# Kernel tuning notes

Measured on AMD Instinct MI355X. Metric: run time of the kernel, lower is better.

The kernel has to match this reference:

```python
import jax, jax.numpy as jnp
import numpy as np

H, W, C, E = 6, 40, 512, 128  # hardcoded in module


def setup_inputs() -> dict:
    key = jax.random.key(0)
    ks = jax.random.split(key, 9)
    nB = 512
    inp = {
        "prev_hidden": jax.random.normal(ks[0], (nB, C), jnp.float32),
        "conv_feats": jax.random.normal(ks[1], (nB, C, H, W), jnp.float32),
        "conv_feats_origin": jax.random.normal(ks[2], (nB, C, H, W), jnp.float32),
        "cur_embeddings": jax.random.normal(ks[3], (nB, E), jnp.float32),
        # params
        "score_w": jax.random.normal(ks[4], (C,), jnp.float32) * (1.0 / np.sqrt(C)),
        "w_ih": jax.random.normal(ks[5], (3 * C, C + E), jnp.float32) * (1.0 / np.sqrt(C)),
        "w_hh": jax.random.normal(ks[6], (3 * C, C), jnp.float32) * (1.0 / np.sqrt(C)),
        "b_ih": jax.random.normal(ks[7], (3 * C,), jnp.float32) * 0.01,
        "b_hh": jax.random.normal(ks[8], (3 * C,), jnp.float32) * 0.01,
    }
    return inp


def gru_cell(x, h, w_ih, w_hh, b_ih, b_hh):
    # PyTorch GRUCell semantics
    gi = x @ w_ih.T + b_ih            # [B, 3C]
    gh = h @ w_hh.T + b_hh            # [B, 3C]
    i_r, i_z, i_n = jnp.split(gi, 3, axis=1)
    h_r, h_z, h_n = jnp.split(gh, 3, axis=1)
    r = jax.nn.sigmoid(i_r + h_r)
    z = jax.nn.sigmoid(i_z + h_z)
    n = jnp.tanh(i_n + r * h_n)
    return (1.0 - z) * n + z * h


def reference(prev_hidden, conv_feats, conv_feats_origin, cur_embeddings,
              score_w, w_ih, w_hh, b_ih, b_hh):
    nB = prev_hidden.shape[0]
    cf = conv_feats.reshape(nB, C, H * W)          # [B, C, HW]
    cfo = conv_feats_origin.reshape(nB, C, H * W)  # [B, C, HW]
    # additive attention score: tanh(feat + h) . score_w
    e = jnp.tanh(cf + prev_hidden[:, :, None])      # [B, C, HW]
    emition = jnp.einsum('bch,c->bh', e, score_w)   # [B, HW]
    alpha = jax.nn.softmax(emition, axis=1)         # softmax over HW positions
    context = jnp.einsum('bch,bh->bc', cfo, alpha)  # [B, C]
    x = jnp.concatenate([context, cur_embeddings], axis=1)  # [B, C+E]
    cur_hidden = gru_cell(x, prev_hidden, w_ih, w_hh, b_ih, b_hh)
    return cur_hidden, alpha.T  # alpha returned as [HW, B] like the original
```

## Files before the change

### kernel.cpp

```cpp
#include <hip/hip_runtime.h>
#include <hip/hip_bf16.h>

#define B   512
#define C   512
#define HW  240
#define E   128
#define XD  640
#define G3  1536

typedef short  s8v  __attribute__((ext_vector_type(8)));
typedef float  f4v  __attribute__((ext_vector_type(4)));

__device__ __forceinline__ float fast_tanh(float x) {
    float ex = __expf(2.0f * x);
    return (ex - 1.0f) * __builtin_amdgcn_rcpf(ex + 1.0f);
}
__device__ __forceinline__ float fast_sigmoid(float x) {
    return __builtin_amdgcn_rcpf(1.0f + __expf(-x));
}
__device__ __forceinline__ unsigned short f2bf(float x) {
    return __builtin_bit_cast(unsigned short, __float2bfloat16(x));
}
__device__ __forceinline__ s8v pack8(float4 a, float4 b) {
    s8v o;
    o[0] = (short)f2bf(a.x); o[1] = (short)f2bf(a.y);
    o[2] = (short)f2bf(a.z); o[3] = (short)f2bf(a.w);
    o[4] = (short)f2bf(b.x); o[5] = (short)f2bf(b.y);
    o[6] = (short)f2bf(b.z); o[7] = (short)f2bf(b.w);
    return o;
}

__global__ __launch_bounds__(256) void emition_kernel(
    const float* __restrict__ prev_hidden,
    const float* __restrict__ conv_feats,
    const float* __restrict__ score_w,
    float* __restrict__ partials)
{
    const int b = blockIdx.x;
    const int chunk = blockIdx.y;
    const int c0 = chunk * 64;
    const int t = threadIdx.x;

    __shared__ float ph_s[64], sw_s[64];
    __shared__ float4 red[4 * 60];

    if (t < 64) {
        ph_s[t] = prev_hidden[b * C + c0 + t];
        sw_s[t] = score_w[c0 + t];
    }
    __syncthreads();

    if (t < 240) {
        const int cs = t / 60;
        const int i  = t % 60;
        const float4* base =
            (const float4*)(conv_feats + ((size_t)(b * C + c0 + cs * 16)) * HW) + i;
        float4 acc = {0.f, 0.f, 0.f, 0.f};
        #pragma unroll
        for (int j = 0; j < 16; ++j) {
            float4 v = base[j * (HW / 4)];
            float ph = ph_s[cs * 16 + j];
            float sw = sw_s[cs * 16 + j];
            acc.x += fast_tanh(v.x + ph) * sw;
            acc.y += fast_tanh(v.y + ph) * sw;
            acc.z += fast_tanh(v.z + ph) * sw;
            acc.w += fast_tanh(v.w + ph) * sw;
        }
        red[cs * 60 + i] = acc;
    }
    __syncthreads();

    if (t < 60) {
        float4 a = red[t], b4 = red[60 + t], c4 = red[120 + t], d4 = red[180 + t];
        float4 s;
        s.x = a.x + b4.x + c4.x + d4.x;
        s.y = a.y + b4.y + c4.y + d4.y;
        s.z = a.z + b4.z + c4.z + d4.z;
        s.w = a.w + b4.w + c4.w + d4.w;
        ((float4*)(partials + ((size_t)b * 8 + chunk) * HW))[t] = s;
    }
}

__global__ __launch_bounds__(256) void ctx_softmax_kernel(
    const float* __restrict__ partials,
    const float* __restrict__ cfo,
    const float* __restrict__ cur_emb,
    float* __restrict__ alpha_out,
    unsigned short* __restrict__ x_bf16)
{
    const int b = blockIdx.x, chunk = blockIdx.y, t = threadIdx.x;
    const int lane = t & 63, w = t >> 6;
    __shared__ float4 af4[60];
    __shared__ float red[4];

    float e = -1e30f;
    if (t < HW) {
        const float* p = partials + (size_t)b * 8 * HW + t;
        float s0 = 0.f;
        #pragma unroll
        for (int k = 0; k < 8; ++k) s0 += p[k * HW];
        e = s0;
    }
    float m = e;
    #pragma unroll
    for (int off = 32; off >= 1; off >>= 1) m = fmaxf(m, __shfl_xor(m, off));
    if (lane == 0) red[w] = m;
    __syncthreads();
    m = fmaxf(fmaxf(red[0], red[1]), fmaxf(red[2], red[3]));

    float p = (t < HW) ? __expf(e - m) : 0.f;
    float s = p;
    #pragma unroll
    for (int off = 32; off >= 1; off >>= 1) s += __shfl_xor(s, off);
    __syncthreads();
    if (lane == 0) red[w] = s;
    __syncthreads();
    s = red[0] + red[1] + red[2] + red[3];
    float inv = __builtin_amdgcn_rcpf(s);
    float a = p * inv;

    if (t < HW) ((float*)af4)[t] = a;
    if (chunk == 0) {
        if (t < HW) alpha_out[(size_t)t * B + b] = a;
        if (t < E)  x_bf16[(size_t)b * XD + C + t] = f2bf(cur_emb[b * E + t]);
    }
    __syncthreads();

    const int r = chunk * 64 + w * 16 + (lane >> 2);
    const int q = lane & 3;
    const float4* row = (const float4*)(cfo + ((size_t)(b * C + r)) * HW);

    float acc = 0.f;
    #pragma unroll
    for (int k = 0; k < 15; ++k) {
        float4 v = row[q + 4 * k];
        float4 av = af4[q + 4 * k];
        acc += v.x * av.x + v.y * av.y + v.z * av.z + v.w * av.w;
    }
    acc += __shfl_xor(acc, 1);
    acc += __shfl_xor(acc, 2);
    if (q == 0) x_bf16[(size_t)b * XD + r] = f2bf(acc);
}

__global__ __launch_bounds__(256) void gemm_kernel(
    const unsigned short* __restrict__ x,
    const float* __restrict__ hprev,
    const float* __restrict__ wih,
    const float* __restrict__ whh,
    const float* __restrict__ b_ih, const float* __restrict__ b_hh,
    float* __restrict__ gi, float* __restrict__ gh)
{
    const int z = blockIdx.z;
    const float* Wmat = z ? whh : wih;
    const float* bias = z ? b_hh : b_ih;
    float* out = z ? gh : gi;
    const int K = z ? C : XD;

    const int b0 = blockIdx.x * 64;
    const int j0 = blockIdx.y * 64;

    __shared__ alignas(16) unsigned short As[64][72];
    __shared__ alignas(16) unsigned short Ws[64][72];

    const int t = threadIdx.x, lane = t & 63, w = t >> 6;
    const int wm = w & 1, wn = w >> 1;
    const int r = t >> 2, col0 = (t & 3) * 16;
    const int q = lane >> 4, mm = lane & 15;

    f4v z4 = {0.f, 0.f, 0.f, 0.f};
    f4v acc[2][2] = {{z4, z4}, {z4, z4}};

    for (int k0 = 0; k0 < K; k0 += 64) {
        s8v a0, a1, w0, w1;
        if (z) {
            const float4* pa = (const float4*)&hprev[(size_t)(b0 + r) * C + k0 + col0];
            float4 f0 = pa[0], f1 = pa[1], f2 = pa[2], f3 = pa[3];
            a0 = pack8(f0, f1); a1 = pack8(f2, f3);
        } else {
            const unsigned short* pa = &x[(size_t)(b0 + r) * XD + k0 + col0];
            a0 = *(const s8v*)pa; a1 = *(const s8v*)(pa + 8);
        }
        {
            const float4* pw = (const float4*)&Wmat[(size_t)(j0 + r) * K + k0 + col0];
            float4 f0 = pw[0], f1 = pw[1], f2 = pw[2], f3 = pw[3];
            w0 = pack8(f0, f1); w1 = pack8(f2, f3);
        }
        __syncthreads();
        *(s8v*)&As[r][col0]     = a0;
        *(s8v*)&As[r][col0 + 8] = a1;
        *(s8v*)&Ws[r][col0]     = w0;
        *(s8v*)&Ws[r][col0 + 8] = w1;
        __syncthreads();

        #pragma unroll
        for (int kk = 0; kk < 2; ++kk) {
            s8v av0 = *(const s8v*)&As[wm * 32 + mm][kk * 32 + q * 8];
            s8v av1 = *(const s8v*)&As[wm * 32 + 16 + mm][kk * 32 + q * 8];
            s8v wv0 = *(const s8v*)&Ws[wn * 32 + mm][kk * 32 + q * 8];
            s8v wv1 = *(const s8v*)&Ws[wn * 32 + 16 + mm][kk * 32 + q * 8];
            acc[0][0] = __builtin_amdgcn_mfma_f32_16x16x32_bf16(av0, wv0, acc[0][0], 0, 0, 0);
            acc[0][1] = __builtin_amdgcn_mfma_f32_16x16x32_bf16(av0, wv1, acc[0][1], 0, 0, 0);
            acc[1][0] = __builtin_amdgcn_mfma_f32_16x16x32_bf16(av1, wv0, acc[1][0], 0, 0, 0);
            acc[1][1] = __builtin_amdgcn_mfma_f32_16x16x32_bf16(av1, wv1, acc[1][1], 0, 0, 0);
        }
    }

    #pragma unroll
    for (int mi = 0; mi < 2; ++mi)
        #pragma unroll
        for (int ni = 0; ni < 2; ++ni) {
            int jj = j0 + wn * 32 + ni * 16 + mm;
            float bv = bias[jj];
            #pragma unroll
            for (int rg = 0; rg < 4; ++rg) {
                int bi = b0 + wm * 32 + mi * 16 + q * 4 + rg;
                out[(size_t)bi * G3 + jj] = acc[mi][ni][rg] + bv;
            }
        }
}

__global__ void gates_kernel(const float* __restrict__ gi,
                             const float* __restrict__ gh,
                             const float* __restrict__ hprev,
                             float* __restrict__ out)
{
    int idx = blockIdx.x * blockDim.x + threadIdx.x;
    if (idx >= B * C) return;
    int b = idx >> 9;
    int c = idx & 511;
    const float* gib = gi + (size_t)b * G3;
    const float* ghb = gh + (size_t)b * G3;
    float r  = fast_sigmoid(gib[c] + ghb[c]);
    float zz = fast_sigmoid(gib[c + C] + ghb[c + C]);
    float n  = fast_tanh(gib[c + 2 * C] + r * ghb[c + 2 * C]);
    out[idx] = (1.f - zz) * n + zz * hprev[idx];
}

extern "C" void kernel_launch(void* const* d_in, const int* in_sizes, int n_in,
                              void* d_out, int out_size, void* d_ws, size_t ws_size,
                              hipStream_t stream)
{
    const float* prev_hidden = (const float*)d_in[0];
    const float* conv_feats  = (const float*)d_in[1];
    const float* cfo         = (const float*)d_in[2];
    const float* emb         = (const float*)d_in[3];
    const float* score_w     = (const float*)d_in[4];
    const float* w_ih        = (const float*)d_in[5];
    const float* w_hh        = (const float*)d_in[6];
    const float* b_ih        = (const float*)d_in[7];
    const float* b_hh        = (const float*)d_in[8];

    float* out       = (float*)d_out;
    float* alpha_out = out + B * C;

    char* ws = (char*)d_ws;
    float* partials          = (float*)(ws);
    float* gi                = (float*)(ws);
    float* gh                = (float*)(ws + 3932160);
    unsigned short* x_bf16   = (unsigned short*)(ws + 7077888);

    emition_kernel<<<dim3(B, 8), 256, 0, stream>>>(prev_hidden, conv_feats, score_w, partials);
    ctx_softmax_kernel<<<dim3(B, 8), 256, 0, stream>>>(partials, cfo, emb, alpha_out, x_bf16);
    gemm_kernel<<<dim3(8, 24, 2), 256, 0, stream>>>(x_bf16, prev_hidden, w_ih, w_hh,
                                                    b_ih, b_hh, gi, gh);
    gates_kernel<<<(B * C + 255) / 256, 256, 0, stream>>>(gi, gh, prev_hidden, out);
}
```

Baseline: 518.6 us.

## Fuse emition and softmax-context kernels into one per-batch attention kernel

Merges the score kernel and the softmax/context kernel into a single 512-thread block per batch row, so the partial-score round trip through global memory and one launch are removed. The tanh-dot is rewritten algebraically as a sum of -2*sw/(exp(2x+2h)+1), dropping the constant term, which softmax cancels, and a subtract per element. Each block now handles all 512 channels, giving 512 blocks instead of 4096, which lowers parallelism per launch and may cut memory-level parallelism on the bandwidth-bound reads of conv_feats and cfo.

```diff
diff --git a/kernel.cpp b/kernel.cpp
--- a/kernel.cpp
+++ b/kernel.cpp
@@ -4,6 +4,7 @@
 #define B   512
 #define C   512
 #define HW  240
+#define HW4 60
 #define E   128
 #define XD  640
 #define G3  1536
@@ -30,116 +31,107 @@
     return o;
 }
 
-__global__ __launch_bounds__(256) void emition_kernel(
+__global__ __launch_bounds__(512) void attn_kernel(
     const float* __restrict__ prev_hidden,
     const float* __restrict__ conv_feats,
-    const float* __restrict__ score_w,
-    float* __restrict__ partials)
-{
-    const int b = blockIdx.x;
-    const int chunk = blockIdx.y;
-    const int c0 = chunk * 64;
-    const int t = threadIdx.x;
-
-    __shared__ float ph_s[64], sw_s[64];
-    __shared__ float4 red[4 * 60];
-
-    if (t < 64) {
-        ph_s[t] = prev_hidden[b * C + c0 + t];
-        sw_s[t] = score_w[c0 + t];
-    }
-    __syncthreads();
-
-    if (t < 240) {
-        const int cs = t / 60;
-        const int i  = t % 60;
-        const float4* base =
-            (const float4*)(conv_feats + ((size_t)(b * C + c0 + cs * 16)) * HW) + i;
-        float4 acc = {0.f, 0.f, 0.f, 0.f};
-        #pragma unroll
-        for (int j = 0; j < 16; ++j) {
-            float4 v = base[j * (HW / 4)];
-            float ph = ph_s[cs * 16 + j];
-            float sw = sw_s[cs * 16 + j];
-            acc.x += fast_tanh(v.x + ph) * sw;
-            acc.y += fast_tanh(v.y + ph) * sw;
-            acc.z += fast_tanh(v.z + ph) * sw;
-            acc.w += fast_tanh(v.w + ph) * sw;
-        }
-        red[cs * 60 + i] = acc;
-    }
-    __syncthreads();
-
-    if (t < 60) {
-        float4 a = red[t], b4 = red[60 + t], c4 = red[120 + t], d4 = red[180 + t];
-        float4 s;
-        s.x = a.x + b4.x + c4.x + d4.x;
-        s.y = a.y + b4.y + c4.y + d4.y;
-        s.z = a.z + b4.z + c4.z + d4.z;
-        s.w = a.w + b4.w + c4.w + d4.w;
-        ((float4*)(partials + ((size_t)b * 8 + chunk) * HW))[t] = s;
-    }
-}
-
-__global__ __launch_bounds__(256) void ctx_softmax_kernel(
-    const float* __restrict__ partials,
     const float* __restrict__ cfo,
     const float* __restrict__ cur_emb,
+    const float* __restrict__ score_w,
     float* __restrict__ alpha_out,
     unsigned short* __restrict__ x_bf16)
 {
-    const int b = blockIdx.x, chunk = blockIdx.y, t = threadIdx.x;
-    const int lane = t & 63, w = t >> 6;
-    __shared__ float4 af4[60];
-    __shared__ float red[4];
-
-    float e = -1e30f;
-    if (t < HW) {
-        const float* p = partials + (size_t)b * 8 * HW + t;
-        float s0 = 0.f;
-        #pragma unroll
-        for (int k = 0; k < 8; ++k) s0 += p[k * HW];
-        e = s0;
-    }
-    float m = e;
+    const int b    = blockIdx.x;
+    const int t    = threadIdx.x;
+    const int w    = t >> 6;
+    const int lane = t & 63;
+
+    __shared__ float ph2_s[C];
+    __shared__ float msw_s[C];
+    __shared__ f4v   red[8][HW4];
+    __shared__ f4v   af4[HW4];
+
+    ph2_s[t] = 2.0f * prev_hidden[(size_t)b * C + t];
+    msw_s[t] = -2.0f * score_w[t];
+    if (t < E) x_bf16[(size_t)b * XD + C + t] = f2bf(cur_emb[(size_t)b * E + t]);
+    __syncthreads();
+
+    {
+        const int g = w;
+        const int i = lane;
+        f4v acc = {0.f, 0.f, 0.f, 0.f};
+        if (i < HW4) {
+            const float4* cf4 = (const float4*)conv_feats
+                              + (size_t)(b * C + g * 64) * HW4 + i;
+            #pragma unroll 8
+            for (int j = 0; j < 64; ++j) {
+                float4 v  = cf4[(size_t)j * HW4];
+                float ph2 = ph2_s[g * 64 + j];
+                float msw = msw_s[g * 64 + j];
+                acc[0] += msw * __builtin_amdgcn_rcpf(__expf(fmaf(v.x, 2.0f, ph2)) + 1.0f);
+                acc[1] += msw * __builtin_amdgcn_rcpf(__expf(fmaf(v.y, 2.0f, ph2)) + 1.0f);
+                acc[2] += msw * __builtin_amdgcn_rcpf(__expf(fmaf(v.z, 2.0f, ph2)) + 1.0f);
+                acc[3] += msw * __builtin_amdgcn_rcpf(__expf(fmaf(v.w, 2.0f, ph2)) + 1.0f);
+            }
+            red[g][i] = acc;
+        }
+    }
+    __syncthreads();
+
+    if (w == 0) {
+        const bool act = lane < HW4;
+        f4v e4 = {0.f, 0.f, 0.f, 0.f};
+        if (act) {
+            #pragma unroll
+            for (int g = 0; g < 8; ++g) {
+                f4v r = red[g][lane];
+                e4[0] += r[0]; e4[1] += r[1]; e4[2] += r[2]; e4[3] += r[3];
+            }
+        }
+        float mx = act ? fmaxf(fmaxf(e4[0], e4[1]), fmaxf(e4[2], e4[3])) : -1e30f;
+        #pragma unroll
+        for (int off = 32; off >= 1; off >>= 1) mx = fmaxf(mx, __shfl_xor(mx, off));
+
+        f4v p4;
+        p4[0] = act ? __expf(e4[0] - mx) : 0.f;
+        p4[1] = act ? __expf(e4[1] - mx) : 0.f;
+        p4[2] = act ? __expf(e4[2] - mx) : 0.f;
+        p4[3] = act ? __expf(e4[3] - mx) : 0.f;
+        float s = p4[0] + p4[1] + p4[2] + p4[3];
+        #pragma unroll
+        for (int off = 32; off >= 1; off >>= 1) s += __shfl_xor(s, off);
+        float inv = __builtin_amdgcn_rcpf(s);
+
+        if (act) {
+            f4v a;
+            a[0] = p4[0] * inv; a[1] = p4[1] * inv;
+            a[2] = p4[2] * inv; a[3] = p4[3] * inv;
+            af4[lane] = a;
+            float* ao = alpha_out + b;
+            ao[(size_t)(4 * lane + 0) * B] = a[0];
+            ao[(size_t)(4 * lane + 1) * B] = a[1];
+            ao[(size_t)(4 * lane + 2) * B] = a[2];
+            ao[(size_t)(4 * lane + 3) * B] = a[3];
+        }
+    }
+    __syncthreads();
+
+    const int r0 = (w << 4) + (lane >> 2);
+    const int q  = lane & 3;
     #pragma unroll
-    for (int off = 32; off >= 1; off >>= 1) m = fmaxf(m, __shfl_xor(m, off));
-    if (lane == 0) red[w] = m;
-    __syncthreads();
-    m = fmaxf(fmaxf(red[0], red[1]), fmaxf(red[2], red[3]));
-
-    float p = (t < HW) ? __expf(e - m) : 0.f;
-    float s = p;
-    #pragma unroll
-    for (int off = 32; off >= 1; off >>= 1) s += __shfl_xor(s, off);
-    __syncthreads();
-    if (lane == 0) red[w] = s;
-    __syncthreads();
-    s = red[0] + red[1] + red[2] + red[3];
-    float inv = __builtin_amdgcn_rcpf(s);
-    float a = p * inv;
-
-    if (t < HW) ((float*)af4)[t] = a;
-    if (chunk == 0) {
-        if (t < HW) alpha_out[(size_t)t * B + b] = a;
-        if (t < E)  x_bf16[(size_t)b * XD + C + t] = f2bf(cur_emb[b * E + t]);
-    }
-    __syncthreads();
-
-    const int r = chunk * 64 + w * 16 + (lane >> 2);
-    const int q = lane & 3;
-    const float4* row = (const float4*)(cfo + ((size_t)(b * C + r)) * HW);
-
-    float acc = 0.f;
-    #pragma unroll
-    for (int k = 0; k < 15; ++k) {
-        float4 v = row[q + 4 * k];
-        float4 av = af4[q + 4 * k];
-        acc += v.x * av.x + v.y * av.y + v.z * av.z + v.w * av.w;
-    }
-    acc += __shfl_xor(acc, 1);
-    acc += __shfl_xor(acc, 2);
-    if (q == 0) x_bf16[(size_t)b * XD + r] = f2bf(acc);
+    for (int p = 0; p < 4; ++p) {
+        const int r = p * 128 + r0;
+        const float4* row = (const float4*)cfo + (size_t)(b * C + r) * HW4;
+        float acc = 0.f;
+        #pragma unroll
+        for (int k = 0; k < 15; ++k) {
+            float4 v = row[q + 4 * k];
+            f4v   av = af4[q + 4 * k];
+            acc += v.x * av[0] + v.y * av[1] + v.z * av[2] + v.w * av[3];
+        }
+        acc += __shfl_xor(acc, 1);
+        acc += __shfl_xor(acc, 2);
+        if (q == 0) x_bf16[(size_t)b * XD + r] = f2bf(acc);
+    }
 }
 
 __global__ __launch_bounds__(256) void gemm_kernel(
@@ -254,13 +246,12 @@
     float* alpha_out = out + B * C;
 
     char* ws = (char*)d_ws;
-    float* partials          = (float*)(ws);
-    float* gi                = (float*)(ws);
-    float* gh                = (float*)(ws + 3932160);
-    unsigned short* x_bf16   = (unsigned short*)(ws + 7077888);
-
-    emition_kernel<<<dim3(B, 8), 256, 0, stream>>>(prev_hidden, conv_feats, score_w, partials);
-    ctx_softmax_kernel<<<dim3(B, 8), 256, 0, stream>>>(partials, cfo, emb, alpha_out, x_bf16);
+    float* gi              = (float*)(ws);
+    float* gh              = (float*)(ws + 3145728);
+    unsigned short* x_bf16 = (unsigned short*)(ws + 6291456);
+
+    attn_kernel<<<dim3(B), 512, 0, stream>>>(prev_hidden, conv_feats, cfo, emb,
+                                             score_w, alpha_out, x_bf16);
     gemm_kernel<<<dim3(8, 24, 2), 256, 0, stream>>>(x_bf16, prev_hidden, w_ih, w_hh,
                                                     b_ih, b_hh, gi, gh);
     gates_kernel<<<(B * C + 255) / 256, 256, 0, stream>>>(gi, gh, prev_hidden, out);
```

Result: no change. 515.8 us (-0.5%).
